# Kernel tuning notes

Hardware: AMD Instinct MI355X
Metric: run time of the kernel (lower is better)

The kernel has to match this reference:

```python
import jax, jax.numpy as jnp
import numpy as np


def setup_inputs() -> dict:
    key = jax.random.key(0)
    k1, k2, k3, k4 = jax.random.split(key, 4)
    N, C, H, W = 4, 256, 64, 64
    Co, kh, kw, dg = 256, 3, 3, 1
    x = jax.random.normal(k1, (N, C, H, W), dtype=jnp.float32)
    offset = jax.random.normal(k2, (N, 2 * dg * kh * kw, H, W), dtype=jnp.float32)
    mask = jax.random.uniform(k3, (N, dg * kh * kw, H, W), dtype=jnp.float32)
    weight = jax.random.normal(k4, (Co, C, kh, kw), dtype=jnp.float32) * 0.02
    bias = jnp.zeros((Co,), dtype=jnp.float32)
    return {"x": x, "offset": offset, "mask": mask, "weight": weight, "bias": bias,
            "stride": 1, "padding": 1, "dilation": 1, "deformable_groups": 1}


def _dcn_v2(x, offset, mask, weight, bias, stride, padding, dilation, dg):
    N, C, H, W = x.shape
    Co, Ci, kh, kw = weight.shape
    K = kh * kw
    Ho, Wo = offset.shape[2], offset.shape[3]
    Cg = C // dg

    off = offset.reshape(N, dg, K, 2, Ho, Wo)
    dy, dx = off[:, :, :, 0], off[:, :, :, 1]          # [N,dg,K,Ho,Wo]
    m = mask.reshape(N, dg, K, Ho, Wo)

    ki = (jnp.arange(K) // kw).astype(jnp.float32)      # kernel row index
    kj = (jnp.arange(K) % kw).astype(jnp.float32)       # kernel col index
    base_y = (jnp.arange(Ho, dtype=jnp.float32) * stride - padding)
    base_x = (jnp.arange(Wo, dtype=jnp.float32) * stride - padding)
    # sampling coordinates [N,dg,K,Ho,Wo]
    py = dy + base_y[None, None, None, :, None] + (ki * dilation)[None, None, :, None, None]
    px = dx + base_x[None, None, None, None, :] + (kj * dilation)[None, None, :, None, None]

    y0 = jnp.floor(py)
    x0 = jnp.floor(px)
    wy1 = py - y0
    wx1 = px - x0
    wy0 = 1.0 - wy1
    wx0 = 1.0 - wx1
    y0i = y0.astype(jnp.int32)
    x0i = x0.astype(jnp.int32)

    xr = x.reshape(N, dg, Cg, H * W)

    def gather(yi, xi):
        valid = ((yi >= 0) & (yi < H) & (xi >= 0) & (xi < W)).astype(x.dtype)
        idx = jnp.clip(yi, 0, H - 1) * W + jnp.clip(xi, 0, W - 1)   # [N,dg,K,Ho,Wo]
        flat = idx.reshape(N, dg, 1, K * Ho * Wo)
        g = jnp.take_along_axis(xr, flat, axis=-1).reshape(N, dg, Cg, K, Ho, Wo)
        return g * valid[:, :, None]

    sampled = (gather(y0i, x0i) * (wy0 * wx0)[:, :, None]
               + gather(y0i, x0i + 1) * (wy0 * wx1)[:, :, None]
               + gather(y0i + 1, x0i) * (wy1 * wx0)[:, :, None]
               + gather(y0i + 1, x0i + 1) * (wy1 * wx1)[:, :, None])
    sampled = sampled * m[:, :, None]                     # modulation
    sampled = sampled.reshape(N, C, K, Ho, Wo)

    out = jnp.einsum('nckhw,ock->nohw', sampled, weight.reshape(Co, C, K))
    return out + bias[None, :, None, None]


def reference(x, offset, mask, weight, bias, stride, padding, dilation, deformable_groups):
    return _dcn_v2(x, offset, mask, weight, bias, stride, padding, dilation, deformable_groups)
```

## Files before the change

kernel.cpp:

```cpp
#include <hip/hip_runtime.h>


typedef _Float16 f16x8 __attribute__((ext_vector_type(8)));
typedef _Float16 f16x4 __attribute__((ext_vector_type(4)));
typedef float f32x4 __attribute__((ext_vector_type(4)));

#define C_IN 256
#define CO   256
#define KK   9
#define HWSZ 4096
#define LDB  40
#define BUFB (64 * LDB)
#define PSTR (4 * CO * HWSZ)

struct __align__(16) SP2 { uint4 off; f16x4 w; };

static __device__ __forceinline__ f16x8 splat8(_Float16 v) {
    f16x8 r = {v, v, v, v, v, v, v, v};
    return r;
}

__global__ void transpose_x_kernel(const float* __restrict__ x,
                                   _Float16* __restrict__ xt) {
    __shared__ float tile[64][65];
    const int n  = blockIdx.z;
    const int p0 = blockIdx.x * 64;
    const int c0 = blockIdx.y * 64;
    const int tx = threadIdx.x & 63;
    const int ty = threadIdx.x >> 6;
    for (int i = 0; i < 16; ++i) {
        int c = ty * 16 + i;
        tile[c][tx] = x[((size_t)(n * C_IN + c0 + c) << 12) + p0 + tx];
    }
    __syncthreads();
    for (int i = 0; i < 16; ++i) {
        int p = ty * 16 + i;
        xt[((size_t)((n << 12) + p0 + p) << 8) + c0 + tx] = (_Float16)tile[tx][p];
    }
}

__global__ void transpose_w_kernel(const float* __restrict__ w,
                                   _Float16* __restrict__ wt2) {
    const int o = blockIdx.x;
    const int c = threadIdx.x;
    const int f = o >> 4, r = o & 15, cc = c >> 5, kq = c & 31;
    for (int kk = 0; kk < KK; ++kk) {
        int q = cc * 9 + kk;
        wt2[((f * 72 + q) * 16 + r) * 32 + kq] =
            (_Float16)w[(o * C_IN + c) * KK + kk];
    }
}

template <int NQ>
__launch_bounds__(256, 3)
__global__ void dcn_main_kernel(const float* __restrict__ offset,
                                const float* __restrict__ mask,
                                const float* __restrict__ bias,
                                const _Float16* __restrict__ xt,
                                const _Float16* __restrict__ wt2,
                                float* __restrict__ out,
                                _Float16* __restrict__ parts) {
    constexpr int TPB = 9 / NQ;
    constexpr int NS  = 8 * TPB;
    __shared__ SP2 sP[64 * TPB];
    __shared__ _Float16 sB[2 * BUFB];

    const int tid = threadIdx.x;
    const int nwg = 256 * NQ;
    const int cpx = nwg >> 3;
    const int lin = blockIdx.x;
    const int id  = (lin & 7) * cpx + (lin >> 3);
    const int q3  = (NQ > 1) ? (id >> 8) : 0;
    const int pt  = id & 255;
    const int p0   = pt * 64;
    const int n    = p0 >> 12;
    const int phw0 = p0 & 4095;

    for (int t = tid; t < 64 * TPB; t += 256) {
        int pl = t / TPB;
        int tl = t - pl * TPB;
        int k  = q3 * TPB + tl;
        int phw = phw0 + pl;
        int h = phw >> 6, w = phw & 63;
        float dy = offset[(size_t)(n * 18 + 2 * k)     * HWSZ + phw];
        float dx = offset[(size_t)(n * 18 + 2 * k + 1) * HWSZ + phw];
        float mv = mask  [(size_t)(n * 9 + k)          * HWSZ + phw];
        float py = dy + (float)(h - 1 + k / 3);
        float px = dx + (float)(w - 1 + k % 3);
        float y0f = floorf(py), x0f = floorf(px);
        int y0 = (int)y0f, x0 = (int)x0f;
        float wy1 = py - y0f, wx1 = px - x0f;
        float wy0 = 1.f - wy1, wx0 = 1.f - wx1;
        int y1 = y0 + 1, x1 = x0 + 1;
        float vy0 = (y0 >= 0 && y0 < 64) ? 1.f : 0.f;
        float vy1 = (y1 >= 0 && y1 < 64) ? 1.f : 0.f;
        float vx0 = (x0 >= 0 && x0 < 64) ? 1.f : 0.f;
        float vx1 = (x1 >= 0 && x1 < 64) ? 1.f : 0.f;
        int cy0 = min(max(y0, 0), 63), cy1 = min(max(y1, 0), 63);
        int cx0 = min(max(x0, 0), 63), cx1 = min(max(x1, 0), 63);
        SP2 e;
        e.off = make_uint4((unsigned)(cy0 * 64 + cx0) << 9,
                           (unsigned)(cy0 * 64 + cx1) << 9,
                           (unsigned)(cy1 * 64 + cx0) << 9,
                           (unsigned)(cy1 * 64 + cx1) << 9);
        f16x4 wv;
        wv.x = (_Float16)(wy0 * wx0 * mv * vy0 * vx0);
        wv.y = (_Float16)(wy0 * wx1 * mv * vy0 * vx1);
        wv.z = (_Float16)(wy1 * wx0 * mv * vy1 * vx0);
        wv.w = (_Float16)(wy1 * wx1 * mv * vy1 * vx1);
        e.w = wv;
        sP[t] = e;
    }
    __syncthreads();

    const int lane = tid & 63;
    const int wid  = tid >> 6;
    const int l15  = lane & 15;
    const int lhi  = lane >> 4;

    const int pixl = tid >> 2;
    const int oct  = tid & 3;
    const int pixT = pixl * TPB;

    const char* xb  = (const char*)(xt + ((size_t)n << 12) * C_IN);
    const char* wtb = (const char*)wt2;

    const int vBe = l15 * LDB + lhi * 8;
    const int vWe = pixl * LDB + oct * 8;
    const unsigned chBase = (unsigned)(oct * 16);

    unsigned voffA[4];
    for (int fm = 0; fm < 4; ++fm) {
        int fglob = wid * 4 + fm;
        voffA[fm] = (unsigned)((fglob * 72 + q3 * TPB) * 1024
                               + l15 * 64 + lhi * 16);
    }

    f16x8 ga[2][4];
    f16x8 aa[2][4];
    f16x4 gw[2];
    f32x4 acc[4][4];
    for (int i = 0; i < 4; ++i)
        for (int j = 0; j < 4; ++j)
            acc[i][j] = (f32x4){0.f, 0.f, 0.f, 0.f};

#define ISSUE_GA(T, SLOT)                                                     \
    {                                                                         \
        const SP2 e_ = sP[pixT + (T) % TPB];                                  \
        gw[SLOT] = e_.w;                                                      \
        const unsigned c_ = chBase + (unsigned)(((T) / TPB) * 64);            \
        ga[SLOT][0] = *(const f16x8*)(xb + (e_.off.x + c_));                  \
        ga[SLOT][1] = *(const f16x8*)(xb + (e_.off.y + c_));                  \
        ga[SLOT][2] = *(const f16x8*)(xb + (e_.off.z + c_));                  \
        ga[SLOT][3] = *(const f16x8*)(xb + (e_.off.w + c_));                  \
    }

#define ISSUE_A(T, SLOT)                                                      \
    {                                                                         \
        const unsigned qo_ = (unsigned)((((T) / TPB) * 9 + (T) % TPB) * 1024);\
        aa[SLOT][0] = *(const f16x8*)(wtb + voffA[0] + qo_);                  \
        aa[SLOT][1] = *(const f16x8*)(wtb + voffA[1] + qo_);                  \
        aa[SLOT][2] = *(const f16x8*)(wtb + voffA[2] + qo_);                  \
        aa[SLOT][3] = *(const f16x8*)(wtb + voffA[3] + qo_);                  \
    }

#define COMBINE(SLOT, BUF)                                                    \
    {                                                                         \
        _Float16* bw_ = &sB[0] + (BUF) * BUFB + vWe;                          \
        f16x8 r_ = ga[SLOT][0] * splat8(gw[SLOT].x)                           \
                 + ga[SLOT][1] * splat8(gw[SLOT].y)                           \
                 + ga[SLOT][2] * splat8(gw[SLOT].z)                           \
                 + ga[SLOT][3] * splat8(gw[SLOT].w);                          \
        *(f16x8*)(bw_) = r_;                                                  \
    }

#define MFMA_STEP(SLOT, BUF)                                                  \
    {                                                                         \
        const _Float16* br_ = &sB[0] + (BUF) * BUFB + vBe;                    \
        __builtin_amdgcn_s_setprio(1);                                        \
        for (int fn_ = 0; fn_ < 4; ++fn_) {                                   \
            f16x8 b_ = *(const f16x8*)(br_ + fn_ * 16 * LDB);                 \
            for (int fm_ = 0; fm_ < 4; ++fm_)                                 \
                acc[fm_][fn_] = __builtin_amdgcn_mfma_f32_16x16x32_f16(       \
                    aa[SLOT][fm_], b_, acc[fm_][fn_], 0, 0, 0);               \
        }                                                                     \
        __builtin_amdgcn_s_setprio(0);                                        \
    }

#define BAR()                                                                 \
    {                                                                         \
        asm volatile("s_waitcnt lgkmcnt(0)" ::: "memory");                    \
        __builtin_amdgcn_s_barrier();                                         \
        asm volatile("" ::: "memory");                                        \
    }

    ISSUE_GA(0, 0)
    ISSUE_GA(1, 1)
    ISSUE_A(0, 0)
    COMBINE(0, 0)
    BAR()

#pragma unroll
    for (int s = 0; s < NS; ++s) {
        if (s + 1 < NS) ISSUE_A(s + 1, (s + 1) & 1)
        if (s + 2 < NS) ISSUE_GA(s + 2, s & 1)
        __builtin_amdgcn_sched_barrier(0);
        MFMA_STEP(s & 1, s & 1)
        if (s + 1 < NS) {
            COMBINE((s + 1) & 1, (s + 1) & 1)
            BAR()
        }
    }

    if constexpr (NQ > 1) {
        _Float16* pp = parts + (size_t)q3 * PSTR;
        for (int fm = 0; fm < 4; ++fm)
            for (int fn = 0; fn < 4; ++fn) {
                int pix = phw0 + fn * 16 + l15;
                for (int r = 0; r < 4; ++r) {
                    int o = wid * 64 + fm * 16 + lhi * 4 + r;
                    pp[((size_t)(n * CO + o) << 12) + pix] =
                        (_Float16)acc[fm][fn][r];
                }
            }
    } else {
        for (int fm = 0; fm < 4; ++fm)
            for (int fn = 0; fn < 4; ++fn) {
                int pix = phw0 + fn * 16 + l15;
                for (int r = 0; r < 4; ++r) {
                    int o = wid * 64 + fm * 16 + lhi * 4 + r;
                    out[((size_t)(n * CO + o) << 12) + pix] =
                        acc[fm][fn][r] + bias[o];
                }
            }
    }
#undef ISSUE_GA
#undef ISSUE_A
#undef COMBINE
#undef MFMA_STEP
#undef BAR
}

__global__ void reduce_kernel(float* __restrict__ out,
                              const _Float16* __restrict__ parts,
                              const float* __restrict__ bias, int n8) {
    int i = blockIdx.x * blockDim.x + threadIdx.x;
    if (i >= n8) return;
    f16x8 a = ((const f16x8*)parts)[i];
    f16x8 b = ((const f16x8*)(parts + (size_t)PSTR))[i];
    f16x8 c = ((const f16x8*)(parts + 2 * (size_t)PSTR))[i];
    float bv = bias[((i * 8) >> 12) & 255];
    f32x4 r0, r1;
    for (int e = 0; e < 4; ++e)
        r0[e] = (float)a[e] + (float)b[e] + (float)c[e] + bv;
    for (int e = 0; e < 4; ++e)
        r1[e] = (float)a[e + 4] + (float)b[e + 4] + (float)c[e + 4] + bv;
    ((f32x4*)out)[2 * i]     = r0;
    ((f32x4*)out)[2 * i + 1] = r1;
}

extern "C" void kernel_launch(void* const* d_in, const int* in_sizes, int n_in,
                              void* d_out, int out_size, void* d_ws, size_t ws_size,
                              hipStream_t stream) {
    const float* x      = (const float*)d_in[0];
    const float* offset = (const float*)d_in[1];
    const float* mask   = (const float*)d_in[2];
    const float* weight = (const float*)d_in[3];
    const float* bias   = (const float*)d_in[4];
    float* out = (float*)d_out;

    _Float16* xt  = (_Float16*)d_ws;
    _Float16* wt2 = (_Float16*)((char*)d_ws + 8388608);
    _Float16* parts = (_Float16*)((char*)d_ws + 9568256);
    const bool split = ws_size >= (size_t)9568256 + (size_t)3 * PSTR * 2;

    transpose_x_kernel<<<dim3(64, 4, 4), 256, 0, stream>>>(x, xt);
    transpose_w_kernel<<<CO, C_IN, 0, stream>>>(weight, wt2);
    if (split) {
        dcn_main_kernel<3><<<dim3(768), 256, 0, stream>>>(offset, mask, bias,
                                                          xt, wt2, out, parts);
        reduce_kernel<<<dim3(PSTR / 8 / 256), 256, 0, stream>>>(out, parts, bias,
                                                                PSTR / 8);
    } else {
        dcn_main_kernel<1><<<dim3(256), 256, 0, stream>>>(offset, mask, bias,
                                                          xt, wt2, out, parts);
    }
}
```

Baseline: 54.07 us.

## Warp-specialize DCN main kernel into gather producer and MFMA consumer waves

```diff
diff --git a/kernel.cpp b/kernel.cpp
--- a/kernel.cpp
+++ b/kernel.cpp
@@ -51,8 +51,8 @@
     }
 }
 
-template <int NQ>
-__launch_bounds__(256, 3)
+template <int NHALF>
+__launch_bounds__(512, 2)
 __global__ void dcn_main_kernel(const float* __restrict__ offset,
                                 const float* __restrict__ mask,
                                 const float* __restrict__ bias,
@@ -60,26 +60,25 @@
                                 const _Float16* __restrict__ wt2,
                                 float* __restrict__ out,
                                 _Float16* __restrict__ parts) {
-    constexpr int TPB = 9 / NQ;
-    constexpr int NS  = 8 * TPB;
-    __shared__ SP2 sP[64 * TPB];
+    constexpr int NS = 72 / NHALF;
+    __shared__ SP2 sP[576];
     __shared__ _Float16 sB[2 * BUFB];
 
     const int tid = threadIdx.x;
-    const int nwg = 256 * NQ;
+    const int nwg = 256 * NHALF;
     const int cpx = nwg >> 3;
     const int lin = blockIdx.x;
     const int id  = (lin & 7) * cpx + (lin >> 3);
-    const int q3  = (NQ > 1) ? (id >> 8) : 0;
-    const int pt  = id & 255;
+    const int half = (NHALF > 1) ? (id >> 8) : 0;
+    const int pt   = id & 255;
     const int p0   = pt * 64;
     const int n    = p0 >> 12;
     const int phw0 = p0 & 4095;
-
-    for (int t = tid; t < 64 * TPB; t += 256) {
-        int pl = t / TPB;
-        int tl = t - pl * TPB;
-        int k  = q3 * TPB + tl;
+    const int cc0  = half * (8 / NHALF);
+
+    for (int t = tid; t < 576; t += 512) {
+        int pl = t / 9;
+        int k  = t - pl * 9;
         int phw = phw0 + pl;
         int h = phw >> 6, w = phw & 63;
         float dy = offset[(size_t)(n * 18 + 2 * k)     * HWSZ + phw];
@@ -113,65 +112,42 @@
     }
     __syncthreads();
 
-    const int lane = tid & 63;
-    const int wid  = tid >> 6;
-    const int l15  = lane & 15;
-    const int lhi  = lane >> 4;
-
-    const int pixl = tid >> 2;
-    const int oct  = tid & 3;
-    const int pixT = pixl * TPB;
-
-    const char* xb  = (const char*)(xt + ((size_t)n << 12) * C_IN);
-    const char* wtb = (const char*)wt2;
-
-    const int vBe = l15 * LDB + lhi * 8;
-    const int vWe = pixl * LDB + oct * 8;
-    const unsigned chBase = (unsigned)(oct * 16);
-
-    unsigned voffA[4];
-    for (int fm = 0; fm < 4; ++fm) {
-        int fglob = wid * 4 + fm;
-        voffA[fm] = (unsigned)((fglob * 72 + q3 * TPB) * 1024
-                               + l15 * 64 + lhi * 16);
-    }
-
-    f16x8 ga[2][4];
-    f16x8 aa[2][4];
-    f16x4 gw[2];
-    f32x4 acc[4][4];
-    for (int i = 0; i < 4; ++i)
-        for (int j = 0; j < 4; ++j)
-            acc[i][j] = (f32x4){0.f, 0.f, 0.f, 0.f};
-
-#define ISSUE_GA(T, SLOT)                                                     \
-    {                                                                         \
-        const SP2 e_ = sP[pixT + (T) % TPB];                                  \
-        gw[SLOT] = e_.w;                                                      \
-        const unsigned c_ = chBase + (unsigned)(((T) / TPB) * 64);            \
-        ga[SLOT][0] = *(const f16x8*)(xb + (e_.off.x + c_));                  \
-        ga[SLOT][1] = *(const f16x8*)(xb + (e_.off.y + c_));                  \
-        ga[SLOT][2] = *(const f16x8*)(xb + (e_.off.z + c_));                  \
-        ga[SLOT][3] = *(const f16x8*)(xb + (e_.off.w + c_));                  \
-    }
+    const int wid = tid >> 6;
+
+#define BAR()                                                                 \
+    {                                                                         \
+        asm volatile("s_waitcnt lgkmcnt(0)" ::: "memory");                    \
+        __builtin_amdgcn_s_barrier();                                         \
+        asm volatile("" ::: "memory");                                        \
+    }
+
+    if (wid < 4) {
+        const int lane = tid & 63;
+        const int l15  = lane & 15;
+        const int lhi  = lane >> 4;
+        const char* wtb = (const char*)wt2;
+        const int vBe = l15 * LDB + lhi * 8;
+
+        unsigned voffA[4];
+        for (int fm = 0; fm < 4; ++fm) {
+            int fglob = wid * 4 + fm;
+            voffA[fm] = (unsigned)((fglob * 72 + cc0 * 9) * 1024
+                                   + l15 * 64 + lhi * 16);
+        }
+
+        f16x8 aa[2][4];
+        f32x4 acc[4][4];
+        for (int i = 0; i < 4; ++i)
+            for (int j = 0; j < 4; ++j)
+                acc[i][j] = (f32x4){0.f, 0.f, 0.f, 0.f};
 
 #define ISSUE_A(T, SLOT)                                                      \
     {                                                                         \
-        const unsigned qo_ = (unsigned)((((T) / TPB) * 9 + (T) % TPB) * 1024);\
+        const unsigned qo_ = (unsigned)((T) * 1024);                          \
         aa[SLOT][0] = *(const f16x8*)(wtb + voffA[0] + qo_);                  \
         aa[SLOT][1] = *(const f16x8*)(wtb + voffA[1] + qo_);                  \
         aa[SLOT][2] = *(const f16x8*)(wtb + voffA[2] + qo_);                  \
         aa[SLOT][3] = *(const f16x8*)(wtb + voffA[3] + qo_);                  \
-    }
-
-#define COMBINE(SLOT, BUF)                                                    \
-    {                                                                         \
-        _Float16* bw_ = &sB[0] + (BUF) * BUFB + vWe;                          \
-        f16x8 r_ = ga[SLOT][0] * splat8(gw[SLOT].x)                           \
-                 + ga[SLOT][1] * splat8(gw[SLOT].y)                           \
-                 + ga[SLOT][2] * splat8(gw[SLOT].z)                           \
-                 + ga[SLOT][3] * splat8(gw[SLOT].w);                          \
-        *(f16x8*)(bw_) = r_;                                                  \
     }
 
 #define MFMA_STEP(SLOT, BUF)                                                  \
@@ -187,57 +163,87 @@
         __builtin_amdgcn_s_setprio(0);                                        \
     }
 
-#define BAR()                                                                 \
-    {                                                                         \
-        asm volatile("s_waitcnt lgkmcnt(0)" ::: "memory");                    \
-        __builtin_amdgcn_s_barrier();                                         \
-        asm volatile("" ::: "memory");                                        \
-    }
-
-    ISSUE_GA(0, 0)
-    ISSUE_GA(1, 1)
-    ISSUE_A(0, 0)
-    COMBINE(0, 0)
-    BAR()
-
+        ISSUE_A(0, 0)
+        BAR()
 #pragma unroll
-    for (int s = 0; s < NS; ++s) {
-        if (s + 1 < NS) ISSUE_A(s + 1, (s + 1) & 1)
-        if (s + 2 < NS) ISSUE_GA(s + 2, s & 1)
-        __builtin_amdgcn_sched_barrier(0);
-        MFMA_STEP(s & 1, s & 1)
-        if (s + 1 < NS) {
-            COMBINE((s + 1) & 1, (s + 1) & 1)
+        for (int s = 0; s < NS; ++s) {
+            if (s + 1 < NS) ISSUE_A(s + 1, (s + 1) & 1)
+            __builtin_amdgcn_sched_barrier(0);
+            MFMA_STEP(s & 1, s & 1)
             BAR()
         }
-    }
-
-    if constexpr (NQ > 1) {
-        _Float16* pp = parts + (size_t)q3 * PSTR;
-        for (int fm = 0; fm < 4; ++fm)
-            for (int fn = 0; fn < 4; ++fn) {
-                int pix = phw0 + fn * 16 + l15;
-                for (int r = 0; r < 4; ++r) {
-                    int o = wid * 64 + fm * 16 + lhi * 4 + r;
-                    pp[((size_t)(n * CO + o) << 12) + pix] =
-                        (_Float16)acc[fm][fn][r];
+
+        if constexpr (NHALF > 1) {
+            _Float16* pp = parts + (size_t)half * PSTR;
+            for (int fm = 0; fm < 4; ++fm)
+                for (int fn = 0; fn < 4; ++fn) {
+                    int pix = phw0 + fn * 16 + l15;
+                    for (int r = 0; r < 4; ++r) {
+                        int o = wid * 64 + fm * 16 + lhi * 4 + r;
+                        pp[((size_t)(n * CO + o) << 12) + pix] =
+                            (_Float16)acc[fm][fn][r];
+                    }
                 }
-            }
+        } else {
+            for (int fm = 0; fm < 4; ++fm)
+                for (int fn = 0; fn < 4; ++fn) {
+                    int pix = phw0 + fn * 16 + l15;
+                    for (int r = 0; r < 4; ++r) {
+                        int o = wid * 64 + fm * 16 + lhi * 4 + r;
+                        out[((size_t)(n * CO + o) << 12) + pix] =
+                            acc[fm][fn][r] + bias[o];
+                    }
+                }
+        }
+#undef ISSUE_A
+#undef MFMA_STEP
     } else {
-        for (int fm = 0; fm < 4; ++fm)
-            for (int fn = 0; fn < 4; ++fn) {
-                int pix = phw0 + fn * 16 + l15;
-                for (int r = 0; r < 4; ++r) {
-                    int o = wid * 64 + fm * 16 + lhi * 4 + r;
-                    out[((size_t)(n * CO + o) << 12) + pix] =
-                        acc[fm][fn][r] + bias[o];
-                }
-            }
-    }
+        const int tid2 = tid - 256;
+        const int pixl = tid2 >> 2;
+        const int oct  = tid2 & 3;
+        const int pixT = pixl * 9;
+        const char* xb = (const char*)(xt + ((size_t)n << 12) * C_IN);
+        const int vWe = pixl * LDB + oct * 8;
+        const unsigned chBase = (unsigned)(oct * 16 + cc0 * 64);
+
+        f16x8 ga[2][4];
+        f16x4 gw[2];
+
+#define ISSUE_GA(T, SLOT)                                                     \
+    {                                                                         \
+        const SP2 e_ = sP[pixT + (T) % 9];                                    \
+        gw[SLOT] = e_.w;                                                      \
+        const unsigned c_ = chBase + (unsigned)(((T) / 9) * 64);              \
+        ga[SLOT][0] = *(const f16x8*)(xb + (e_.off.x + c_));                  \
+        ga[SLOT][1] = *(const f16x8*)(xb + (e_.off.y + c_));                  \
+        ga[SLOT][2] = *(const f16x8*)(xb + (e_.off.z + c_));                  \
+        ga[SLOT][3] = *(const f16x8*)(xb + (e_.off.w + c_));                  \
+    }
+
+#define COMBINE(SLOT, BUF)                                                    \
+    {                                                                         \
+        _Float16* bw_ = &sB[0] + (BUF) * BUFB + vWe;                          \
+        f16x8 r_ = ga[SLOT][0] * splat8(gw[SLOT].x)                           \
+                 + ga[SLOT][1] * splat8(gw[SLOT].y)                           \
+                 + ga[SLOT][2] * splat8(gw[SLOT].z)                           \
+                 + ga[SLOT][3] * splat8(gw[SLOT].w);                          \
+        *(f16x8*)(bw_) = r_;                                                  \
+    }
+
+        ISSUE_GA(0, 0)
+        ISSUE_GA(1, 1)
+        COMBINE(0, 0)
+        BAR()
+#pragma unroll
+        for (int s = 0; s < NS; ++s) {
+            if (s + 2 < NS) ISSUE_GA(s + 2, s & 1)
+            __builtin_amdgcn_sched_barrier(0);
+            if (s + 1 < NS) COMBINE((s + 1) & 1, (s + 1) & 1)
+            BAR()
+        }
 #undef ISSUE_GA
-#undef ISSUE_A
 #undef COMBINE
-#undef MFMA_STEP
+    }
 #undef BAR
 }
 
@@ -248,13 +254,12 @@
     if (i >= n8) return;
     f16x8 a = ((const f16x8*)parts)[i];
     f16x8 b = ((const f16x8*)(parts + (size_t)PSTR))[i];
-    f16x8 c = ((const f16x8*)(parts + 2 * (size_t)PSTR))[i];
     float bv = bias[((i * 8) >> 12) & 255];
     f32x4 r0, r1;
     for (int e = 0; e < 4; ++e)
-        r0[e] = (float)a[e] + (float)b[e] + (float)c[e] + bv;
+        r0[e] = (float)a[e] + (float)b[e] + bv;
     for (int e = 0; e < 4; ++e)
-        r1[e] = (float)a[e + 4] + (float)b[e + 4] + (float)c[e + 4] + bv;
+        r1[e] = (float)a[e + 4] + (float)b[e + 4] + bv;
     ((f32x4*)out)[2 * i]     = r0;
     ((f32x4*)out)[2 * i + 1] = r1;
 }
@@ -272,17 +277,17 @@
     _Float16* xt  = (_Float16*)d_ws;
     _Float16* wt2 = (_Float16*)((char*)d_ws + 8388608);
     _Float16* parts = (_Float16*)((char*)d_ws + 9568256);
-    const bool split = ws_size >= (size_t)9568256 + (size_t)3 * PSTR * 2;
+    const bool split = ws_size >= (size_t)9568256 + (size_t)2 * PSTR * 2;
 
     transpose_x_kernel<<<dim3(64, 4, 4), 256, 0, stream>>>(x, xt);
     transpose_w_kernel<<<CO, C_IN, 0, stream>>>(weight, wt2);
     if (split) {
-        dcn_main_kernel<3><<<dim3(768), 256, 0, stream>>>(offset, mask, bias,
+        dcn_main_kernel<2><<<dim3(512), 512, 0, stream>>>(offset, mask, bias,
                                                           xt, wt2, out, parts);
         reduce_kernel<<<dim3(PSTR / 8 / 256), 256, 0, stream>>>(out, parts, bias,
                                                                 PSTR / 8);
     } else {
-        dcn_main_kernel<1><<<dim3(256), 256, 0, stream>>>(offset, mask, bias,
+        dcn_main_kernel<1><<<dim3(256), 512, 0, stream>>>(offset, mask, bias,
                                                           xt, wt2, out, parts);
     }
 }
```

Result: no change. 53.67 us (-0.7%).

## Use 256-pixel, 1024-thread tiles with shared-memory weight staging and 4-way K split

Applied to the files above, without the earlier changes.

```diff
diff --git a/kernel.cpp b/kernel.cpp
--- a/kernel.cpp
+++ b/kernel.cpp
@@ -10,10 +10,11 @@
 #define KK   9
 #define HWSZ 4096
 #define LDB  40
-#define BUFB (64 * LDB)
+#define BUFB (256 * LDB)
+#define BUFA (256 * LDB)
 #define PSTR (4 * CO * HWSZ)
 
-struct __align__(16) SP2 { uint4 off; f16x4 w; };
+struct __align__(16) SPX { ushort4 cell; f16x4 w; };
 
 static __device__ __forceinline__ f16x8 splat8(_Float16 v) {
     f16x8 r = {v, v, v, v, v, v, v, v};
@@ -40,46 +41,46 @@
 }
 
 __global__ void transpose_w_kernel(const float* __restrict__ w,
-                                   _Float16* __restrict__ wt2) {
+                                   _Float16* __restrict__ wt3) {
     const int o = blockIdx.x;
     const int c = threadIdx.x;
     const int f = o >> 4, r = o & 15, cc = c >> 5, kq = c & 31;
     for (int kk = 0; kk < KK; ++kk) {
         int q = cc * 9 + kk;
-        wt2[((f * 72 + q) * 16 + r) * 32 + kq] =
+        wt3[((q * 16 + f) * 16 + r) * 32 + kq] =
             (_Float16)w[(o * C_IN + c) * KK + kk];
     }
 }
 
 template <int NQ>
-__launch_bounds__(256, 3)
+__launch_bounds__(1024, 1)
 __global__ void dcn_main_kernel(const float* __restrict__ offset,
                                 const float* __restrict__ mask,
                                 const float* __restrict__ bias,
                                 const _Float16* __restrict__ xt,
-                                const _Float16* __restrict__ wt2,
+                                const _Float16* __restrict__ wt3,
                                 float* __restrict__ out,
                                 _Float16* __restrict__ parts) {
-    constexpr int TPB = 9 / NQ;
-    constexpr int NS  = 8 * TPB;
-    __shared__ SP2 sP[64 * TPB];
+    constexpr int NS = 72 / NQ;
+    __shared__ SPX sP[2304];
     __shared__ _Float16 sB[2 * BUFB];
+    __shared__ _Float16 sA[2 * BUFA];
 
     const int tid = threadIdx.x;
-    const int nwg = 256 * NQ;
+    const int nwg = 64 * NQ;
     const int cpx = nwg >> 3;
     const int lin = blockIdx.x;
     const int id  = (lin & 7) * cpx + (lin >> 3);
-    const int q3  = (NQ > 1) ? (id >> 8) : 0;
-    const int pt  = id & 255;
-    const int p0   = pt * 64;
+    const int quarter = (NQ > 1) ? (id >> 6) : 0;
+    const int pt   = id & 63;
+    const int p0   = pt * 256;
     const int n    = p0 >> 12;
     const int phw0 = p0 & 4095;
-
-    for (int t = tid; t < 64 * TPB; t += 256) {
-        int pl = t / TPB;
-        int tl = t - pl * TPB;
-        int k  = q3 * TPB + tl;
+    const int q0   = quarter * NS;
+
+    for (int t = tid; t < 2304; t += 1024) {
+        int pl = t / 9;
+        int k  = t - pl * 9;
         int phw = phw0 + pl;
         int h = phw >> 6, w = phw & 63;
         float dy = offset[(size_t)(n * 18 + 2 * k)     * HWSZ + phw];
@@ -98,11 +99,11 @@
         float vx1 = (x1 >= 0 && x1 < 64) ? 1.f : 0.f;
         int cy0 = min(max(y0, 0), 63), cy1 = min(max(y1, 0), 63);
         int cx0 = min(max(x0, 0), 63), cx1 = min(max(x1, 0), 63);
-        SP2 e;
-        e.off = make_uint4((unsigned)(cy0 * 64 + cx0) << 9,
-                           (unsigned)(cy0 * 64 + cx1) << 9,
-                           (unsigned)(cy1 * 64 + cx0) << 9,
-                           (unsigned)(cy1 * 64 + cx1) << 9);
+        SPX e;
+        e.cell = make_ushort4((unsigned short)(cy0 * 64 + cx0),
+                              (unsigned short)(cy0 * 64 + cx1),
+                              (unsigned short)(cy1 * 64 + cx0),
+                              (unsigned short)(cy1 * 64 + cx1));
         f16x4 wv;
         wv.x = (_Float16)(wy0 * wx0 * mv * vy0 * vx0);
         wv.y = (_Float16)(wy0 * wx1 * mv * vy0 * vx1);
@@ -115,74 +116,68 @@
 
     const int lane = tid & 63;
     const int wid  = tid >> 6;
+    const int m    = wid >> 2;
+    const int nq   = wid & 3;
     const int l15  = lane & 15;
     const int lhi  = lane >> 4;
 
-    const int pixl = tid >> 2;
+    const int spix = tid >> 2;
     const int oct  = tid & 3;
-    const int pixT = pixl * TPB;
-
-    const char* xb  = (const char*)(xt + ((size_t)n << 12) * C_IN);
-    const char* wtb = (const char*)wt2;
-
-    const int vBe = l15 * LDB + lhi * 8;
-    const int vWe = pixl * LDB + oct * 8;
-    const unsigned chBase = (unsigned)(oct * 16);
-
-    unsigned voffA[4];
-    for (int fm = 0; fm < 4; ++fm) {
-        int fglob = wid * 4 + fm;
-        voffA[fm] = (unsigned)((fglob * 72 + q3 * TPB) * 1024
-                               + l15 * 64 + lhi * 16);
-    }
-
-    f16x8 ga[2][4];
-    f16x8 aa[2][4];
-    f16x4 gw[2];
+    const int spix9 = spix * 9;
+
+    const char* xb   = (const char*)(xt + ((size_t)n << 12) * C_IN);
+    const char* wt3b = (const char*)wt3 + ((size_t)q0 << 14);
+
+    const int vWe = spix * LDB + oct * 8;
+    const int aWe = (tid >> 2) * LDB + (tid & 3) * 8;
+    const int vBe = (nq * 64 + l15) * LDB + lhi * 8;
+    const int aBe = (m * 64 + l15) * LDB + lhi * 8;
+
+    f16x8 ga[4];
+    uint4 areg;
+    f16x4 gw;
     f32x4 acc[4][4];
     for (int i = 0; i < 4; ++i)
         for (int j = 0; j < 4; ++j)
             acc[i][j] = (f32x4){0.f, 0.f, 0.f, 0.f};
 
-#define ISSUE_GA(T, SLOT)                                                     \
-    {                                                                         \
-        const SP2 e_ = sP[pixT + (T) % TPB];                                  \
-        gw[SLOT] = e_.w;                                                      \
-        const unsigned c_ = chBase + (unsigned)(((T) / TPB) * 64);            \
-        ga[SLOT][0] = *(const f16x8*)(xb + (e_.off.x + c_));                  \
-        ga[SLOT][1] = *(const f16x8*)(xb + (e_.off.y + c_));                  \
-        ga[SLOT][2] = *(const f16x8*)(xb + (e_.off.z + c_));                  \
-        ga[SLOT][3] = *(const f16x8*)(xb + (e_.off.w + c_));                  \
-    }
-
-#define ISSUE_A(T, SLOT)                                                      \
-    {                                                                         \
-        const unsigned qo_ = (unsigned)((((T) / TPB) * 9 + (T) % TPB) * 1024);\
-        aa[SLOT][0] = *(const f16x8*)(wtb + voffA[0] + qo_);                  \
-        aa[SLOT][1] = *(const f16x8*)(wtb + voffA[1] + qo_);                  \
-        aa[SLOT][2] = *(const f16x8*)(wtb + voffA[2] + qo_);                  \
-        aa[SLOT][3] = *(const f16x8*)(wtb + voffA[3] + qo_);                  \
-    }
-
-#define COMBINE(SLOT, BUF)                                                    \
-    {                                                                         \
-        _Float16* bw_ = &sB[0] + (BUF) * BUFB + vWe;                          \
-        f16x8 r_ = ga[SLOT][0] * splat8(gw[SLOT].x)                           \
-                 + ga[SLOT][1] * splat8(gw[SLOT].y)                           \
-                 + ga[SLOT][2] * splat8(gw[SLOT].z)                           \
-                 + ga[SLOT][3] * splat8(gw[SLOT].w);                          \
-        *(f16x8*)(bw_) = r_;                                                  \
-    }
-
-#define MFMA_STEP(SLOT, BUF)                                                  \
-    {                                                                         \
-        const _Float16* br_ = &sB[0] + (BUF) * BUFB + vBe;                    \
+#define ISSUE_GA(T)                                                           \
+    {                                                                         \
+        const SPX e_ = sP[spix9 + (q0 + (T)) % 9];                            \
+        gw = e_.w;                                                            \
+        const unsigned c_ = (unsigned)(((q0 + (T)) / 9) * 64 + oct * 16);     \
+        ga[0] = *(const f16x8*)(xb + (((unsigned)e_.cell.x << 9) + c_));      \
+        ga[1] = *(const f16x8*)(xb + (((unsigned)e_.cell.y << 9) + c_));      \
+        ga[2] = *(const f16x8*)(xb + (((unsigned)e_.cell.z << 9) + c_));      \
+        ga[3] = *(const f16x8*)(xb + (((unsigned)e_.cell.w << 9) + c_));      \
+    }
+
+#define ISSUE_AL(T)                                                           \
+    { areg = *(const uint4*)(wt3b + (((size_t)(T)) << 14) + tid * 16); }
+
+#define COMBINE(BUF)                                                          \
+    {                                                                         \
+        f16x8 r_ = ga[0] * splat8(gw.x) + ga[1] * splat8(gw.y)                \
+                 + ga[2] * splat8(gw.z) + ga[3] * splat8(gw.w);               \
+        *(f16x8*)(&sB[(BUF) * BUFB + vWe]) = r_;                              \
+    }
+
+#define AWRITE(BUF)                                                           \
+    { *(uint4*)(&sA[(BUF) * BUFA + aWe]) = areg; }
+
+#define MFMA_STEP(BUF)                                                        \
+    {                                                                         \
+        const _Float16* ab_ = &sA[(BUF) * BUFA] + aBe;                        \
+        const _Float16* bb_ = &sB[(BUF) * BUFB] + vBe;                        \
+        f16x8 af_[4];                                                         \
+        for (int fm_ = 0; fm_ < 4; ++fm_)                                     \
+            af_[fm_] = *(const f16x8*)(ab_ + fm_ * 16 * LDB);                 \
         __builtin_amdgcn_s_setprio(1);                                        \
         for (int fn_ = 0; fn_ < 4; ++fn_) {                                   \
-            f16x8 b_ = *(const f16x8*)(br_ + fn_ * 16 * LDB);                 \
+            f16x8 b_ = *(const f16x8*)(bb_ + fn_ * 16 * LDB);                 \
             for (int fm_ = 0; fm_ < 4; ++fm_)                                 \
                 acc[fm_][fn_] = __builtin_amdgcn_mfma_f32_16x16x32_f16(       \
-                    aa[SLOT][fm_], b_, acc[fm_][fn_], 0, 0, 0);               \
+                    af_[fm_], b_, acc[fm_][fn_], 0, 0, 0);                    \
         }                                                                     \
         __builtin_amdgcn_s_setprio(0);                                        \
     }
@@ -194,31 +189,34 @@
         asm volatile("" ::: "memory");                                        \
     }
 
-    ISSUE_GA(0, 0)
-    ISSUE_GA(1, 1)
-    ISSUE_A(0, 0)
-    COMBINE(0, 0)
+    ISSUE_AL(0)
+    ISSUE_GA(0)
+    COMBINE(0)
+    AWRITE(0)
     BAR()
 
 #pragma unroll
     for (int s = 0; s < NS; ++s) {
-        if (s + 1 < NS) ISSUE_A(s + 1, (s + 1) & 1)
-        if (s + 2 < NS) ISSUE_GA(s + 2, s & 1)
+        if (s + 1 < NS) {
+            ISSUE_AL(s + 1)
+            ISSUE_GA(s + 1)
+        }
         __builtin_amdgcn_sched_barrier(0);
-        MFMA_STEP(s & 1, s & 1)
+        MFMA_STEP(s & 1)
         if (s + 1 < NS) {
-            COMBINE((s + 1) & 1, (s + 1) & 1)
+            COMBINE((s + 1) & 1)
+            AWRITE((s + 1) & 1)
             BAR()
         }
     }
 
     if constexpr (NQ > 1) {
-        _Float16* pp = parts + (size_t)q3 * PSTR;
+        _Float16* pp = parts + (size_t)quarter * PSTR;
         for (int fm = 0; fm < 4; ++fm)
             for (int fn = 0; fn < 4; ++fn) {
-                int pix = phw0 + fn * 16 + l15;
+                int pix = phw0 + nq * 64 + fn * 16 + l15;
                 for (int r = 0; r < 4; ++r) {
-                    int o = wid * 64 + fm * 16 + lhi * 4 + r;
+                    int o = m * 64 + fm * 16 + lhi * 4 + r;
                     pp[((size_t)(n * CO + o) << 12) + pix] =
                         (_Float16)acc[fm][fn][r];
                 }
@@ -226,17 +224,18 @@
     } else {
         for (int fm = 0; fm < 4; ++fm)
             for (int fn = 0; fn < 4; ++fn) {
-                int pix = phw0 + fn * 16 + l15;
+                int pix = phw0 + nq * 64 + fn * 16 + l15;
                 for (int r = 0; r < 4; ++r) {
-                    int o = wid * 64 + fm * 16 + lhi * 4 + r;
+                    int o = m * 64 + fm * 16 + lhi * 4 + r;
                     out[((size_t)(n * CO + o) << 12) + pix] =
                         acc[fm][fn][r] + bias[o];
                 }
             }
     }
 #undef ISSUE_GA
-#undef ISSUE_A
+#undef ISSUE_AL
 #undef COMBINE
+#undef AWRITE
 #undef MFMA_STEP
 #undef BAR
 }
@@ -249,12 +248,13 @@
     f16x8 a = ((const f16x8*)parts)[i];
     f16x8 b = ((const f16x8*)(parts + (size_t)PSTR))[i];
     f16x8 c = ((const f16x8*)(parts + 2 * (size_t)PSTR))[i];
+    f16x8 d = ((const f16x8*)(parts + 3 * (size_t)PSTR))[i];
     float bv = bias[((i * 8) >> 12) & 255];
     f32x4 r0, r1;
     for (int e = 0; e < 4; ++e)
-        r0[e] = (float)a[e] + (float)b[e] + (float)c[e] + bv;
+        r0[e] = (float)a[e] + (float)b[e] + (float)c[e] + (float)d[e] + bv;
     for (int e = 0; e < 4; ++e)
-        r1[e] = (float)a[e + 4] + (float)b[e + 4] + (float)c[e + 4] + bv;
+        r1[e] = (float)a[e+4] + (float)b[e+4] + (float)c[e+4] + (float)d[e+4] + bv;
     ((f32x4*)out)[2 * i]     = r0;
     ((f32x4*)out)[2 * i + 1] = r1;
 }
@@ -270,19 +270,19 @@
     float* out = (float*)d_out;
 
     _Float16* xt  = (_Float16*)d_ws;
-    _Float16* wt2 = (_Float16*)((char*)d_ws + 8388608);
+    _Float16* wt3 = (_Float16*)((char*)d_ws + 8388608);
     _Float16* parts = (_Float16*)((char*)d_ws + 9568256);
-    const bool split = ws_size >= (size_t)9568256 + (size_t)3 * PSTR * 2;
+    const bool split = ws_size >= (size_t)9568256 + (size_t)4 * PSTR * 2;
 
     transpose_x_kernel<<<dim3(64, 4, 4), 256, 0, stream>>>(x, xt);
-    transpose_w_kernel<<<CO, C_IN, 0, stream>>>(weight, wt2);
+    transpose_w_kernel<<<CO, C_IN, 0, stream>>>(weight, wt3);
     if (split) {
-        dcn_main_kernel<3><<<dim3(768), 256, 0, stream>>>(offset, mask, bias,
-                                                          xt, wt2, out, parts);
+        dcn_main_kernel<4><<<dim3(256), 1024, 0, stream>>>(offset, mask, bias,
+                                                           xt, wt3, out, parts);
         reduce_kernel<<<dim3(PSTR / 8 / 256), 256, 0, stream>>>(out, parts, bias,
                                                                 PSTR / 8);
     } else {
-        dcn_main_kernel<1><<<dim3(256), 256, 0, stream>>>(offset, mask, bias,
-                                                          xt, wt2, out, parts);
-    }
-}
+        dcn_main_kernel<1><<<dim3(64), 1024, 0, stream>>>(offset, mask, bias,
+                                                          xt, wt3, out, parts);
+    }
+}
```

Result: no change. 54.64 us (+1.1%).
